# Optimization experiments

Measured on AMD Instinct MI355X. Metric: run time of the kernel, lower is better.

The kernel has to match this reference:

```python
import jax, jax.numpy as jnp
import numpy as np

LN_EPS = 1e-3

def setup_inputs() -> dict:
    key = jax.random.key(0)
    ks = jax.random.split(key, 3)
    B, H, W, C = 32, 64, 48, 256
    groups = 8
    d = C // groups
    x = jax.random.normal(ks[0], (B, H, W, C), dtype=jnp.float32)
    conv1x1_w = jax.random.normal(ks[1], (d, d), dtype=jnp.float32) * (1.0 / np.sqrt(d))
    conv1x1_b = jnp.zeros((d,), dtype=jnp.float32)
    conv3x3_w = jax.random.normal(ks[2], (3, 3, d, d), dtype=jnp.float32) * (1.0 / np.sqrt(9 * d))
    conv3x3_b = jnp.zeros((d,), dtype=jnp.float32)
    ln_gamma = jnp.ones((d,), dtype=jnp.float32)
    ln_beta = jnp.zeros((d,), dtype=jnp.float32)
    return {"x": x, "conv1x1_w": conv1x1_w, "conv1x1_b": conv1x1_b,
            "conv3x3_w": conv3x3_w, "conv3x3_b": conv3x3_b,
            "ln_gamma": ln_gamma, "ln_beta": ln_beta, "groups": groups}


def reference(x, conv1x1_w, conv1x1_b, conv3x3_w, conv3x3_b, ln_gamma, ln_beta, groups):
    B, H, W, C = x.shape
    g = groups
    d = C // g
    # group split: [B,H,W,C] -> [B*g, H, W, d]
    gx = x.reshape(B, H, W, g, d).transpose(0, 3, 1, 2, 4).reshape(B * g, H, W, d)
    # adaptive pools to (H,1) and (1,W) == mean over W / mean over H
    x_h = gx.mean(axis=2, keepdims=True)                 # [Bg,H,1,d]
    x_w = gx.mean(axis=1, keepdims=True)                 # [Bg,1,W,d]
    hw = jnp.concatenate([x_h, x_w.transpose(0, 2, 1, 3)], axis=1)  # [Bg,H+W,1,d]
    # conv1x1 == per-position linear over channels
    hw = jnp.einsum('bhwd,de->bhwe', hw, conv1x1_w) + conv1x1_b
    xh = jax.nn.sigmoid(hw[:, :H])                       # [Bg,H,1,d]
    xw = jax.nn.sigmoid(hw[:, H:].transpose(0, 2, 1, 3)) # [Bg,1,W,d]
    # LayerNorm over last axis
    y = gx * xh * xw
    mu = y.mean(axis=-1, keepdims=True)
    var = jnp.mean(jnp.square(y - mu), axis=-1, keepdims=True)
    x1 = (y - mu) * jax.lax.rsqrt(var + LN_EPS) * ln_gamma + ln_beta
    # conv3x3 SAME on grouped features
    x2 = jax.lax.conv_general_dilated(
        gx, conv3x3_w, window_strides=(1, 1), padding='SAME',
        dimension_numbers=('NHWC', 'HWIO', 'NHWC')) + conv3x3_b
    # channel softmax of GAP, cross matmuls -> spatial gate
    x11 = jax.nn.softmax(x1.mean(axis=(1, 2)), axis=-1)  # [Bg,d]
    x21 = jax.nn.softmax(x2.mean(axis=(1, 2)), axis=-1)  # [Bg,d]
    w1 = jnp.einsum('bd,bhwd->bhw', x11, x2)
    w2 = jnp.einsum('bd,bhwd->bhw', x21, x1)
    gate = jax.nn.sigmoid((w1 + w2)[..., None])          # [Bg,H,W,1]
    out = gx * gate
    out = out.reshape(B, g, H, W, d).transpose(0, 2, 3, 1, 4).reshape(B, H, W, C)
    return out
```

## Files before the change

### kernel.cpp

```cpp
#include <hip/hip_runtime.h>
#include <math.h>

#define B_ 32
#define H_ 64
#define W_ 48
#define C_ 256
#define G_ 8
#define D_ 32
#define BG_ (B_*G_)
#define LN_EPS_ 1e-3f
#define NPIX_ (H_*W_)

typedef short bf16x8 __attribute__((ext_vector_type(8)));
typedef float f32x4 __attribute__((ext_vector_type(4)));

__device__ __forceinline__ float sigmoidf_(float v) { return 1.0f / (1.0f + expf(-v)); }

__device__ __forceinline__ unsigned short f2bf(float f) {
    unsigned u = __float_as_uint(f);
    u = u + 0x7fffu + ((u >> 16) & 1u);
    return (unsigned short)(u >> 16);
}
__device__ __forceinline__ float bflo(unsigned u) { return __uint_as_float(u << 16); }
__device__ __forceinline__ float bfhi(unsigned u) { return __uint_as_float(u & 0xffff0000u); }

__global__ __launch_bounds__(256) void k0_prep(const float* __restrict__ w3,
                                               unsigned short* __restrict__ wbf)
{
    int i = blockIdx.x * 256 + threadIdx.x;
    if (i < 9 * D_ * D_) {
        int t = i >> 10;
        int rem = i & 1023;
        int e = rem >> 5, d = rem & 31;
        wbf[i] = f2bf(w3[((t << 5) + d) * D_ + e]);
    }
}

__global__ __launch_bounds__(256) void k1_means(const float* __restrict__ x,
                                                const float* __restrict__ w1,
                                                const float* __restrict__ b1,
                                                float* __restrict__ xh,
                                                float* __restrict__ xw)
{
    int bg = blockIdx.x;
    int b = bg >> 3, gi = bg & 7;
    const float* xp = x + (size_t)b * H_ * W_ * C_ + gi * D_;
    __shared__ float mh[H_][D_];
    __shared__ float mw[W_][D_];
    __shared__ float wls[D_ * D_];
    int t = threadIdx.x;
    int c = t & 31;
    int wg = t >> 5;
    for (int i = t; i < D_ * D_; i += 256) wls[i] = w1[i];
    for (int i = t; i < H_ * D_; i += 256) mh[i >> 5][i & 31] = 0.f;
    __syncthreads();

    float colp[6] = {0.f, 0.f, 0.f, 0.f, 0.f, 0.f};
    for (int h = 0; h < H_; ++h) {
        const float* row = xp + (size_t)h * W_ * C_;
        float rp = 0.f;
        #pragma unroll
        for (int j = 0; j < 6; ++j) {
            float v = row[(size_t)(wg * 6 + j) * C_ + c];
            rp += v;
            colp[j] += v;
        }
        rp += __shfl_xor(rp, 32);
        if ((t & 63) < 32) atomicAdd(&mh[h][c], rp);
    }
    #pragma unroll
    for (int j = 0; j < 6; ++j) mw[wg * 6 + j][c] = colp[j] * (1.0f / H_);
    __syncthreads();

    for (int i = t; i < (H_ + W_) * D_; i += 256) {
        int pos = i >> 5, e = i & 31;
        const float* m = (pos < H_) ? mh[pos] : mw[pos - H_];
        float scale = (pos < H_) ? (1.0f / W_) : 1.0f;
        float dot = 0.f;
        #pragma unroll
        for (int d = 0; d < D_; ++d) dot += m[d] * wls[d * D_ + e];
        float s = sigmoidf_(b1[e] + dot * scale);
        if (pos < H_) xh[((size_t)bg * H_ + pos) * D_ + e] = s;
        else          xw[((size_t)bg * W_ + (pos - H_)) * D_ + e] = s;
    }
}

#define SROWS 18
#define SPXL 50
#define ROWB (SPXL * 64)

__global__ __launch_bounds__(256) void k3_conv(const float* __restrict__ x,
                                               const unsigned short* __restrict__ wbf,
                                               const float* __restrict__ b3,
                                               const float* __restrict__ xh,
                                               const float* __restrict__ xw,
                                               const float* __restrict__ gamma,
                                               const float* __restrict__ beta,
                                               unsigned short* __restrict__ x2,
                                               float* __restrict__ s1,
                                               float* __restrict__ s2)
{
    __shared__ unsigned short sbuf[SROWS * SPXL * 32];
    int bi = blockIdx.x;
    int bg = bi >> 2;
    int h0 = (bi & 3) << 4;
    int b = bg >> 3, gi = bg & 7;
    const float* base = x + (size_t)b * H_ * W_ * C_ + gi * D_;
    int t = threadIdx.x;
    int lane = t & 63;
    int wv = t >> 6;

    const int e0 = lane & 15;
    const int ko = (lane >> 4) << 3;
    bf16x8 wf[9][2];
    #pragma unroll
    for (int tp = 0; tp < 9; ++tp)
        #pragma unroll
        for (int n = 0; n < 2; ++n)
            wf[tp][n] = *(const bf16x8*)(const void*)(wbf + (((tp << 5) + (n << 4) + e0) << 5) + ko);
    float be0 = b3[e0], be1 = b3[e0 + 16];

    if (t < SROWS * 2 * 4) {
        int r = t >> 3, side = (t >> 2) & 1, slot = t & 3;
        int px = side ? (SPXL - 1) : 0;
        int addr = r * ROWB + ((((px << 6) + (slot << 4))) ^ ((px & 7) << 4));
        *(uint4*)((char*)sbuf + addr) = make_uint4(0, 0, 0, 0);
    }

    const int NIDX = SROWS * 48 * 8;
    for (int i = t; i < NIDX; i += 256) {
        int r = i / 384;
        int rem = i - r * 384;
        int w = rem >> 3, c4 = rem & 7;
        int hh = h0 - 1 + r;
        unsigned u0 = 0, u1 = 0;
        if (hh >= 0 && hh < H_) {
            float4 v = *(const float4*)(base + ((size_t)hh * W_ + w) * C_ + (c4 << 2));
            u0 = (unsigned)f2bf(v.x) | ((unsigned)f2bf(v.y) << 16);
            u1 = (unsigned)f2bf(v.z) | ((unsigned)f2bf(v.w) << 16);
        }
        int px = w + 1;
        int addr = r * ROWB + ((((px << 6) + (c4 << 3))) ^ ((px & 7) << 4));
        *(uint2*)((char*)sbuf + addr) = make_uint2(u0, u1);
    }
    __syncthreads();

    float s2p0 = 0.f, s2p1 = 0.f;
    for (int q = 0; q < 4; ++q) {
        int r = (wv << 2) + q;
        int h = h0 + r;
        for (int m = 0; m < 3; ++m) {
            int w0 = m << 4;
            f32x4 acc0 = {be0, be0, be0, be0};
            f32x4 acc1 = {be1, be1, be1, be1};
            #pragma unroll
            for (int dh = 0; dh < 3; ++dh) {
                int srow = r + dh;
                #pragma unroll
                for (int dw = 0; dw < 3; ++dw) {
                    int px = w0 + (lane & 15) + dw;
                    int addr = srow * ROWB + ((((px << 6) + ((lane >> 4) << 4))) ^ ((px & 7) << 4));
                    bf16x8 a = *(const bf16x8*)(const void*)((const char*)sbuf + addr);
                    acc0 = __builtin_amdgcn_mfma_f32_16x16x32_bf16(a, wf[dh * 3 + dw][0], acc0, 0, 0, 0);
                    acc1 = __builtin_amdgcn_mfma_f32_16x16x32_bf16(a, wf[dh * 3 + dw][1], acc1, 0, 0, 0);
                }
            }
            #pragma unroll
            for (int rg = 0; rg < 4; ++rg) {
                int pw = w0 + ((lane >> 4) << 2) + rg;
                size_t off = (((size_t)bg * H_ + h) * W_ + pw) * D_;
                x2[off + e0]      = f2bf(acc0[rg]);
                x2[off + e0 + 16] = f2bf(acc1[rg]);
                s2p0 += acc0[rg];
                s2p1 += acc1[rg];
            }
        }
    }
    s2p0 += __shfl_xor(s2p0, 16); s2p0 += __shfl_xor(s2p0, 32);
    s2p1 += __shfl_xor(s2p1, 16); s2p1 += __shfl_xor(s2p1, 32);
    if (lane < 16) {
        atomicAdd(&s2[bg * D_ + e0], s2p0);
        atomicAdd(&s2[bg * D_ + e0 + 16], s2p1);
    }

    float s1p[32];
    #pragma unroll
    for (int c = 0; c < 32; ++c) s1p[c] = 0.f;
    #pragma unroll
    for (int pp = 0; pp < 3; ++pp) {
        int pl = t + (pp << 8);
        int r = pl / 48;
        int w = pl - r * 48;
        int srow = r + 1;
        int px = w + 1;
        float v[32];
        #pragma unroll
        for (int slot = 0; slot < 4; ++slot) {
            int addr = srow * ROWB + ((((px << 6) + (slot << 4))) ^ ((px & 7) << 4));
            uint4 u = *(const uint4*)((const char*)sbuf + addr);
            v[slot * 8 + 0] = bflo(u.x); v[slot * 8 + 1] = bfhi(u.x);
            v[slot * 8 + 2] = bflo(u.y); v[slot * 8 + 3] = bfhi(u.y);
            v[slot * 8 + 4] = bflo(u.z); v[slot * 8 + 5] = bfhi(u.z);
            v[slot * 8 + 6] = bflo(u.w); v[slot * 8 + 7] = bfhi(u.w);
        }
        const float4* ph4 = (const float4*)(xh + (((size_t)bg * H_) + h0 + r) * D_);
        const float4* pw4 = (const float4*)(xw + (((size_t)bg * W_) + w) * D_);
        float y[32];
        float mu = 0.f;
        #pragma unroll
        for (int c4 = 0; c4 < 8; ++c4) {
            float4 a = ph4[c4], bq = pw4[c4];
            y[4 * c4 + 0] = v[4 * c4 + 0] * a.x * bq.x;
            y[4 * c4 + 1] = v[4 * c4 + 1] * a.y * bq.y;
            y[4 * c4 + 2] = v[4 * c4 + 2] * a.z * bq.z;
            y[4 * c4 + 3] = v[4 * c4 + 3] * a.w * bq.w;
            mu += y[4 * c4 + 0] + y[4 * c4 + 1] + y[4 * c4 + 2] + y[4 * c4 + 3];
        }
        mu *= (1.0f / D_);
        float var = 0.f;
        #pragma unroll
        for (int c = 0; c < 32; ++c) { float dl = y[c] - mu; var += dl * dl; }
        var *= (1.0f / D_);
        float rs = rsqrtf(var + LN_EPS_);
        #pragma unroll
        for (int c4 = 0; c4 < 8; ++c4) {
            float4 gq = ((const float4*)gamma)[c4];
            float4 bt = ((const float4*)beta)[c4];
            s1p[4 * c4 + 0] += (y[4 * c4 + 0] - mu) * rs * gq.x + bt.x;
            s1p[4 * c4 + 1] += (y[4 * c4 + 1] - mu) * rs * gq.y + bt.y;
            s1p[4 * c4 + 2] += (y[4 * c4 + 2] - mu) * rs * gq.z + bt.z;
            s1p[4 * c4 + 3] += (y[4 * c4 + 3] - mu) * rs * gq.w + bt.w;
        }
    }
    #pragma unroll
    for (int c = 0; c < 32; ++c) {
        float vv = s1p[c];
        vv += __shfl_xor(vv, 1);  vv += __shfl_xor(vv, 2);  vv += __shfl_xor(vv, 4);
        vv += __shfl_xor(vv, 8);  vv += __shfl_xor(vv, 16); vv += __shfl_xor(vv, 32);
        s1p[c] = vv;
    }
    if (lane == 0) {
        #pragma unroll
        for (int c = 0; c < 32; ++c) atomicAdd(&s1[bg * D_ + c], s1p[c]);
    }
}

__global__ __launch_bounds__(64) void k4_softmax(const float* __restrict__ s1,
                                                 const float* __restrict__ s2,
                                                 float* __restrict__ x11,
                                                 float* __restrict__ x21)
{
    int bg = blockIdx.x;
    int lane = threadIdx.x;
    const float* s = (lane < 32) ? s1 : s2;
    float* o = (lane < 32) ? x11 : x21;
    int c = lane & 31;
    float v = s[bg * D_ + c] * (1.0f / (float)NPIX_);
    float m = v;
    m = fmaxf(m, __shfl_xor(m, 1));  m = fmaxf(m, __shfl_xor(m, 2));
    m = fmaxf(m, __shfl_xor(m, 4));  m = fmaxf(m, __shfl_xor(m, 8));
    m = fmaxf(m, __shfl_xor(m, 16));
    float e = expf(v - m);
    float sm = e;
    sm += __shfl_xor(sm, 1);  sm += __shfl_xor(sm, 2);
    sm += __shfl_xor(sm, 4);  sm += __shfl_xor(sm, 8);
    sm += __shfl_xor(sm, 16);
    o[bg * D_ + c] = e / sm;
}

__global__ __launch_bounds__(192) void k5_final(const float* __restrict__ x,
                                                const float* __restrict__ xh,
                                                const float* __restrict__ xw,
                                                const float* __restrict__ gamma,
                                                const float* __restrict__ beta,
                                                const unsigned short* __restrict__ x2,
                                                const float* __restrict__ x11,
                                                const float* __restrict__ x21,
                                                float* __restrict__ out)
{
    int bi = blockIdx.x;
    int bg = bi >> 4;
    int h0 = (bi & 15) << 2;
    int tid = threadIdx.x;
    int r = tid / W_;
    int w = tid % W_;
    int h = h0 + r;
    int b = bg >> 3, gi = bg & 7;
    size_t pixoff = (size_t)b * H_ * W_ * C_ + ((size_t)h * W_ + w) * C_ + gi * D_;

    const float4* vp  = (const float4*)(x + pixoff);
    const float4* xhp = (const float4*)(xh + ((size_t)bg * H_ + h) * D_);
    const float4* xwp = (const float4*)(xw + ((size_t)bg * W_ + w) * D_);

    float v[D_], y[D_];
    float mu = 0.f;
    #pragma unroll
    for (int q = 0; q < 8; ++q) {
        float4 tq = vp[q], a = xhp[q], bq = xwp[q];
        v[4 * q + 0] = tq.x; v[4 * q + 1] = tq.y; v[4 * q + 2] = tq.z; v[4 * q + 3] = tq.w;
        y[4 * q + 0] = tq.x * a.x * bq.x;
        y[4 * q + 1] = tq.y * a.y * bq.y;
        y[4 * q + 2] = tq.z * a.z * bq.z;
        y[4 * q + 3] = tq.w * a.w * bq.w;
        mu += y[4 * q + 0] + y[4 * q + 1] + y[4 * q + 2] + y[4 * q + 3];
    }
    mu *= (1.0f / D_);
    float var = 0.f;
    #pragma unroll
    for (int c = 0; c < D_; ++c) { float dl = y[c] - mu; var += dl * dl; }
    var *= (1.0f / D_);
    float rs = rsqrtf(var + LN_EPS_);

    const uint4* x2q = (const uint4*)(x2 + (((size_t)bg * H_ + h) * W_ + w) * D_);
    float w1 = 0.f, w2 = 0.f;
    #pragma unroll
    for (int j = 0; j < 4; ++j) {
        uint4 u = x2q[j];
        float xv[8];
        xv[0] = bflo(u.x); xv[1] = bfhi(u.x); xv[2] = bflo(u.y); xv[3] = bfhi(u.y);
        xv[4] = bflo(u.z); xv[5] = bfhi(u.z); xv[6] = bflo(u.w); xv[7] = bfhi(u.w);
        #pragma unroll
        for (int k = 0; k < 8; ++k) {
            int c = j * 8 + k;
            float x1v = (y[c] - mu) * rs * gamma[c] + beta[c];
            w1 += x11[bg * D_ + c] * xv[k];
            w2 += x21[bg * D_ + c] * x1v;
        }
    }
    float gate = sigmoidf_(w1 + w2);

    float4* op = (float4*)(out + pixoff);
    #pragma unroll
    for (int q = 0; q < 8; ++q) {
        float4 tq;
        tq.x = v[4 * q + 0] * gate; tq.y = v[4 * q + 1] * gate;
        tq.z = v[4 * q + 2] * gate; tq.w = v[4 * q + 3] * gate;
        op[q] = tq;
    }
}

extern "C" void kernel_launch(void* const* d_in, const int* in_sizes, int n_in,
                              void* d_out, int out_size, void* d_ws, size_t ws_size,
                              hipStream_t stream)
{
    const float* x     = (const float*)d_in[0];
    const float* w1    = (const float*)d_in[1];
    const float* b1    = (const float*)d_in[2];
    const float* w3    = (const float*)d_in[3];
    const float* b3    = (const float*)d_in[4];
    const float* gamma = (const float*)d_in[5];
    const float* beta  = (const float*)d_in[6];

    char* wsb = (char*)d_ws;
    unsigned short* x2  = (unsigned short*)wsb;
    float* xh  = (float*)(wsb + 50331648);
    float* xw  = (float*)(wsb + 52428800);
    float* s1  = (float*)(wsb + 54001664);
    float* s2  = (float*)(wsb + 54034432);
    float* x11 = (float*)(wsb + 54067200);
    float* x21 = (float*)(wsb + 54099968);
    unsigned short* wbf = (unsigned short*)(wsb + 54132736);

    hipMemsetAsync(s1, 0, 65536, stream);

    k0_prep<<<36, 256, 0, stream>>>(w3, wbf);
    k1_means<<<BG_, 256, 0, stream>>>(x, w1, b1, xh, xw);
    k3_conv<<<BG_ * 4, 256, 0, stream>>>(x, wbf, b3, xh, xw, gamma, beta, x2, s1, s2);
    k4_softmax<<<BG_, 64, 0, stream>>>(s1, s2, x11, x21);
    k5_final<<<BG_ * (H_ / 4), 192, 0, stream>>>(x, xh, xw, gamma, beta, x2, x11, x21,
                                                 (float*)d_out);
}
```

Measured before the change: 343.1 us.

## Stage bf16 copy of input in means kernel and reuse it in conv and final

The means kernel now writes a swizzled bf16 copy of each group's input. It also emits the row and column gates in bf16, using more threads and float4 loads. The conv kernel copies its tiles from that bf16 buffer straight into LDS with global_load_lds, using smaller 8-row tiles and masking at the edges instead of padding. The final kernel reads the bf16 input rather than the fp32 one. This cuts fp32 input reads in the later kernels, but the extra bf16 write costs traffic and the output gating now uses bf16-rounded inputs, which lowers precision.

```diff
diff --git a/kernel.cpp b/kernel.cpp
--- a/kernel.cpp
+++ b/kernel.cpp
@@ -10,6 +10,7 @@
 #define BG_ (B_*G_)
 #define LN_EPS_ 1e-3f
 #define NPIX_ (H_*W_)
+#define XROWB 3072
 
 typedef short bf16x8 __attribute__((ext_vector_type(8)));
 typedef float f32x4 __attribute__((ext_vector_type(4)));
@@ -23,6 +24,10 @@
 }
 __device__ __forceinline__ float bflo(unsigned u) { return __uint_as_float(u << 16); }
 __device__ __forceinline__ float bfhi(unsigned u) { return __uint_as_float(u & 0xffff0000u); }
+
+__device__ __forceinline__ int swz16(int px, int slot) {
+    return ((px << 6) + (slot << 4)) ^ ((px & 7) << 4);
+}
 
 __global__ __launch_bounds__(256) void k0_prep(const float* __restrict__ w3,
                                                unsigned short* __restrict__ wbf)
@@ -36,79 +41,103 @@
     }
 }
 
-__global__ __launch_bounds__(256) void k1_means(const float* __restrict__ x,
+__global__ __launch_bounds__(512) void k1_means(const float* __restrict__ x,
                                                 const float* __restrict__ w1,
                                                 const float* __restrict__ b1,
-                                                float* __restrict__ xh,
-                                                float* __restrict__ xw)
-{
+                                                unsigned short* __restrict__ xbf,
+                                                unsigned short* __restrict__ xhb,
+                                                unsigned short* __restrict__ xwb)
+{
+    __shared__ float mh[H_][D_];
+    __shared__ float mwp[8][W_][D_];
+    __shared__ float wls[D_ * D_];
     int bg = blockIdx.x;
-    int b = bg >> 3, gi = bg & 7;
-    const float* xp = x + (size_t)b * H_ * W_ * C_ + gi * D_;
-    __shared__ float mh[H_][D_];
-    __shared__ float mw[W_][D_];
-    __shared__ float wls[D_ * D_];
-    int t = threadIdx.x;
-    int c = t & 31;
-    int wg = t >> 5;
-    for (int i = t; i < D_ * D_; i += 256) wls[i] = w1[i];
-    for (int i = t; i < H_ * D_; i += 256) mh[i >> 5][i & 31] = 0.f;
-    __syncthreads();
-
-    float colp[6] = {0.f, 0.f, 0.f, 0.f, 0.f, 0.f};
-    for (int h = 0; h < H_; ++h) {
-        const float* row = xp + (size_t)h * W_ * C_;
-        float rp = 0.f;
-        #pragma unroll
-        for (int j = 0; j < 6; ++j) {
-            float v = row[(size_t)(wg * 6 + j) * C_ + c];
-            rp += v;
-            colp[j] += v;
-        }
-        rp += __shfl_xor(rp, 32);
-        if ((t & 63) < 32) atomicAdd(&mh[h][c], rp);
-    }
-    #pragma unroll
-    for (int j = 0; j < 6; ++j) mw[wg * 6 + j][c] = colp[j] * (1.0f / H_);
-    __syncthreads();
-
-    for (int i = t; i < (H_ + W_) * D_; i += 256) {
-        int pos = i >> 5, e = i & 31;
-        const float* m = (pos < H_) ? mh[pos] : mw[pos - H_];
-        float scale = (pos < H_) ? (1.0f / W_) : 1.0f;
-        float dot = 0.f;
-        #pragma unroll
-        for (int d = 0; d < D_; ++d) dot += m[d] * wls[d * D_ + e];
-        float s = sigmoidf_(b1[e] + dot * scale);
-        if (pos < H_) xh[((size_t)bg * H_ + pos) * D_ + e] = s;
-        else          xw[((size_t)bg * W_ + (pos - H_)) * D_ + e] = s;
-    }
-}
-
-#define SROWS 18
-#define SPXL 50
-#define ROWB (SPXL * 64)
-
-__global__ __launch_bounds__(256) void k3_conv(const float* __restrict__ x,
-                                               const unsigned short* __restrict__ wbf,
-                                               const float* __restrict__ b3,
-                                               const float* __restrict__ xh,
-                                               const float* __restrict__ xw,
-                                               const float* __restrict__ gamma,
-                                               const float* __restrict__ beta,
-                                               unsigned short* __restrict__ x2,
-                                               float* __restrict__ s1,
-                                               float* __restrict__ s2)
-{
-    __shared__ unsigned short sbuf[SROWS * SPXL * 32];
-    int bi = blockIdx.x;
-    int bg = bi >> 2;
-    int h0 = (bi & 3) << 4;
     int b = bg >> 3, gi = bg & 7;
     const float* base = x + (size_t)b * H_ * W_ * C_ + gi * D_;
     int t = threadIdx.x;
     int lane = t & 63;
     int wv = t >> 6;
+    int c4 = lane & 7;
+    int pxg = lane >> 3;
+
+    for (int i = t; i < D_ * D_; i += 512) wls[i] = w1[i];
+
+    float4 colp[6];
+    #pragma unroll
+    for (int j = 0; j < 6; ++j) colp[j] = make_float4(0.f, 0.f, 0.f, 0.f);
+
+    for (int i = 0; i < 8; ++i) {
+        int h = (wv << 3) + i;
+        const float* rowp = base + (size_t)h * W_ * C_;
+        char* xrow = (char*)xbf + (((size_t)bg << 6) + h) * XROWB;
+        float4 vj[6];
+        #pragma unroll
+        for (int j = 0; j < 6; ++j)
+            vj[j] = *(const float4*)(rowp + (size_t)(pxg + 8 * j) * C_ + (c4 << 2));
+        float4 rp = make_float4(0.f, 0.f, 0.f, 0.f);
+        #pragma unroll
+        for (int j = 0; j < 6; ++j) {
+            float4 v = vj[j];
+            int px = pxg + 8 * j;
+            unsigned u0 = (unsigned)f2bf(v.x) | ((unsigned)f2bf(v.y) << 16);
+            unsigned u1 = (unsigned)f2bf(v.z) | ((unsigned)f2bf(v.w) << 16);
+            int addr = (((px << 6) + (c4 << 3))) ^ ((px & 7) << 4);
+            *(uint2*)(xrow + addr) = make_uint2(u0, u1);
+            colp[j].x += v.x; colp[j].y += v.y; colp[j].z += v.z; colp[j].w += v.w;
+            rp.x += v.x; rp.y += v.y; rp.z += v.z; rp.w += v.w;
+        }
+        #pragma unroll
+        for (int s = 8; s <= 32; s <<= 1) {
+            rp.x += __shfl_xor(rp.x, s); rp.y += __shfl_xor(rp.y, s);
+            rp.z += __shfl_xor(rp.z, s); rp.w += __shfl_xor(rp.w, s);
+        }
+        if (lane < 8) *(float4*)&mh[h][c4 << 2] = rp;
+    }
+    #pragma unroll
+    for (int j = 0; j < 6; ++j)
+        *(float4*)&mwp[wv][pxg + 8 * j][c4 << 2] = colp[j];
+    __syncthreads();
+
+    for (int i = t; i < W_ * D_; i += 512) {
+        int px = i >> 5, c = i & 31;
+        float s = 0.f;
+        #pragma unroll
+        for (int v = 0; v < 8; ++v) s += mwp[v][px][c];
+        mwp[0][px][c] = s;
+    }
+    __syncthreads();
+
+    for (int i = t; i < (H_ + W_) * D_; i += 512) {
+        int pos = i >> 5, e = i & 31;
+        const float* m = (pos < H_) ? mh[pos] : mwp[0][pos - H_];
+        float scale = (pos < H_) ? (1.0f / W_) : (1.0f / H_);
+        float dot = 0.f;
+        #pragma unroll
+        for (int d = 0; d < D_; ++d) dot += m[d] * wls[d * D_ + e];
+        unsigned short s = f2bf(sigmoidf_(b1[e] + dot * scale));
+        if (pos < H_) xhb[(((size_t)bg << 6) + pos) * D_ + e] = s;
+        else          xwb[((size_t)bg * W_ + (pos - H_)) * D_ + e] = s;
+    }
+}
+
+__global__ __launch_bounds__(256, 4) void k3_conv(const unsigned short* __restrict__ xbf,
+                                                  const unsigned short* __restrict__ wbf,
+                                                  const float* __restrict__ b3,
+                                                  const unsigned short* __restrict__ xhb,
+                                                  const unsigned short* __restrict__ xwb,
+                                                  const float* __restrict__ gamma,
+                                                  const float* __restrict__ beta,
+                                                  unsigned short* __restrict__ x2,
+                                                  float* __restrict__ s1,
+                                                  float* __restrict__ s2)
+{
+    __shared__ unsigned short sbuf[10 * W_ * D_];
+    int bi = blockIdx.x;
+    int bg = bi >> 3;
+    int h0 = (bi & 7) << 3;
+    int t = threadIdx.x;
+    int lane = t & 63;
+    int wv = t >> 6;
 
     const int e0 = lane & 15;
     const int ko = (lane >> 4) << 3;
@@ -120,47 +149,51 @@
             wf[tp][n] = *(const bf16x8*)(const void*)(wbf + (((tp << 5) + (n << 4) + e0) << 5) + ko);
     float be0 = b3[e0], be1 = b3[e0 + 16];
 
-    if (t < SROWS * 2 * 4) {
-        int r = t >> 3, side = (t >> 2) & 1, slot = t & 3;
-        int px = side ? (SPXL - 1) : 0;
-        int addr = r * ROWB + ((((px << 6) + (slot << 4))) ^ ((px & 7) << 4));
-        *(uint4*)((char*)sbuf + addr) = make_uint4(0, 0, 0, 0);
-    }
-
-    const int NIDX = SROWS * 48 * 8;
-    for (int i = t; i < NIDX; i += 256) {
-        int r = i / 384;
-        int rem = i - r * 384;
-        int w = rem >> 3, c4 = rem & 7;
-        int hh = h0 - 1 + r;
-        unsigned u0 = 0, u1 = 0;
-        if (hh >= 0 && hh < H_) {
-            float4 v = *(const float4*)(base + ((size_t)hh * W_ + w) * C_ + (c4 << 2));
-            u0 = (unsigned)f2bf(v.x) | ((unsigned)f2bf(v.y) << 16);
-            u1 = (unsigned)f2bf(v.z) | ((unsigned)f2bf(v.w) << 16);
-        }
-        int px = w + 1;
-        int addr = r * ROWB + ((((px << 6) + (c4 << 3))) ^ ((px & 7) << 4));
-        *(uint2*)((char*)sbuf + addr) = make_uint2(u0, u1);
-    }
+    int sA = (h0 == 0) ? 1 : 0;
+    int sB = (h0 == 56) ? 8 : 9;
+    const char* src = (const char*)xbf + (((size_t)bg << 6) + (h0 - 1 + sA)) * XROWB;
+    char* ldsb = (char*)sbuf + sA * XROWB;
+    int nch = (sB - sA + 1) * 3;
+    for (int ch = wv; ch < nch; ch += 4) {
+        __builtin_amdgcn_global_load_lds(
+            (const __attribute__((address_space(1))) unsigned*)(const void*)(src + (ch << 10) + (lane << 4)),
+            (__attribute__((address_space(3))) unsigned*)(void*)(ldsb + (ch << 10)),
+            16, 0, 0);
+    }
+    if (h0 == 0 && t < 192)  *(uint4*)((char*)sbuf + (t << 4)) = make_uint4(0, 0, 0, 0);
+    if (h0 == 56 && t < 192) *(uint4*)((char*)sbuf + 9 * XROWB + (t << 4)) = make_uint4(0, 0, 0, 0);
     __syncthreads();
 
+    int swz9[9]; bool inv9[9];
+    #pragma unroll
+    for (int m = 0; m < 3; ++m)
+        #pragma unroll
+        for (int dw = 0; dw < 3; ++dw) {
+            int pxi = (m << 4) + (lane & 15) + dw - 1;
+            int pxc = pxi < 0 ? 0 : (pxi > 47 ? 47 : pxi);
+            swz9[m * 3 + dw] = swz16(pxc, lane >> 4);
+            inv9[m * 3 + dw] = (pxi != pxc);
+        }
+    const bf16x8 z8 = {0, 0, 0, 0, 0, 0, 0, 0};
+
     float s2p0 = 0.f, s2p1 = 0.f;
-    for (int q = 0; q < 4; ++q) {
-        int r = (wv << 2) + q;
+    for (int q = 0; q < 2; ++q) {
+        int r = (wv << 1) + q;
         int h = h0 + r;
+        #pragma unroll
         for (int m = 0; m < 3; ++m) {
             int w0 = m << 4;
             f32x4 acc0 = {be0, be0, be0, be0};
             f32x4 acc1 = {be1, be1, be1, be1};
             #pragma unroll
             for (int dh = 0; dh < 3; ++dh) {
-                int srow = r + dh;
+                int srowB = (r + dh) * XROWB;
                 #pragma unroll
                 for (int dw = 0; dw < 3; ++dw) {
-                    int px = w0 + (lane & 15) + dw;
-                    int addr = srow * ROWB + ((((px << 6) + ((lane >> 4) << 4))) ^ ((px & 7) << 4));
-                    bf16x8 a = *(const bf16x8*)(const void*)((const char*)sbuf + addr);
+                    bf16x8 a = *(const bf16x8*)(const void*)((const char*)sbuf + srowB + swz9[m * 3 + dw]);
+                    if ((m == 0 && dw == 0) || (m == 2 && dw == 2)) {
+                        if (inv9[m * 3 + dw]) a = z8;
+                    }
                     acc0 = __builtin_amdgcn_mfma_f32_16x16x32_bf16(a, wf[dh * 3 + dw][0], acc0, 0, 0, 0);
                     acc1 = __builtin_amdgcn_mfma_f32_16x16x32_bf16(a, wf[dh * 3 + dw][1], acc1, 0, 0, 0);
                 }
@@ -186,35 +219,32 @@
     float s1p[32];
     #pragma unroll
     for (int c = 0; c < 32; ++c) s1p[c] = 0.f;
-    #pragma unroll
-    for (int pp = 0; pp < 3; ++pp) {
-        int pl = t + (pp << 8);
-        int r = pl / 48;
-        int w = pl - r * 48;
-        int srow = r + 1;
-        int px = w + 1;
-        float v[32];
-        #pragma unroll
-        for (int slot = 0; slot < 4; ++slot) {
-            int addr = srow * ROWB + ((((px << 6) + (slot << 4))) ^ ((px & 7) << 4));
-            uint4 u = *(const uint4*)((const char*)sbuf + addr);
-            v[slot * 8 + 0] = bflo(u.x); v[slot * 8 + 1] = bfhi(u.x);
-            v[slot * 8 + 2] = bflo(u.y); v[slot * 8 + 3] = bfhi(u.y);
-            v[slot * 8 + 4] = bflo(u.z); v[slot * 8 + 5] = bfhi(u.z);
-            v[slot * 8 + 6] = bflo(u.w); v[slot * 8 + 7] = bfhi(u.w);
-        }
-        const float4* ph4 = (const float4*)(xh + (((size_t)bg * H_) + h0 + r) * D_);
-        const float4* pw4 = (const float4*)(xw + (((size_t)bg * W_) + w) * D_);
+    for (int pl = t; pl < 8 * W_; pl += 256) {
+        int r = pl / W_;
+        int w = pl - r * W_;
+        int srowB = (r + 1) * XROWB;
+        const uint4* ph4 = (const uint4*)(xhb + (((size_t)bg << 6) + h0 + r) * D_);
+        const uint4* pw4 = (const uint4*)(xwb + ((size_t)bg * W_ + w) * D_);
         float y[32];
         float mu = 0.f;
         #pragma unroll
-        for (int c4 = 0; c4 < 8; ++c4) {
-            float4 a = ph4[c4], bq = pw4[c4];
-            y[4 * c4 + 0] = v[4 * c4 + 0] * a.x * bq.x;
-            y[4 * c4 + 1] = v[4 * c4 + 1] * a.y * bq.y;
-            y[4 * c4 + 2] = v[4 * c4 + 2] * a.z * bq.z;
-            y[4 * c4 + 3] = v[4 * c4 + 3] * a.w * bq.w;
-            mu += y[4 * c4 + 0] + y[4 * c4 + 1] + y[4 * c4 + 2] + y[4 * c4 + 3];
+        for (int j = 0; j < 4; ++j) {
+            uint4 uv = *(const uint4*)((const char*)sbuf + srowB + swz16(w, j));
+            uint4 uh = ph4[j];
+            uint4 uw = pw4[j];
+            float vv[8], ah[8], aw[8];
+            vv[0]=bflo(uv.x); vv[1]=bfhi(uv.x); vv[2]=bflo(uv.y); vv[3]=bfhi(uv.y);
+            vv[4]=bflo(uv.z); vv[5]=bfhi(uv.z); vv[6]=bflo(uv.w); vv[7]=bfhi(uv.w);
+            ah[0]=bflo(uh.x); ah[1]=bfhi(uh.x); ah[2]=bflo(uh.y); ah[3]=bfhi(uh.y);
+            ah[4]=bflo(uh.z); ah[5]=bfhi(uh.z); ah[6]=bflo(uh.w); ah[7]=bfhi(uh.w);
+            aw[0]=bflo(uw.x); aw[1]=bfhi(uw.x); aw[2]=bflo(uw.y); aw[3]=bfhi(uw.y);
+            aw[4]=bflo(uw.z); aw[5]=bfhi(uw.z); aw[6]=bflo(uw.w); aw[7]=bfhi(uw.w);
+            #pragma unroll
+            for (int k = 0; k < 8; ++k) {
+                float yy = vv[k] * ah[k] * aw[k];
+                y[j * 8 + k] = yy;
+                mu += yy;
+            }
         }
         mu *= (1.0f / D_);
         float var = 0.f;
@@ -268,9 +298,9 @@
     o[bg * D_ + c] = e / sm;
 }
 
-__global__ __launch_bounds__(192) void k5_final(const float* __restrict__ x,
-                                                const float* __restrict__ xh,
-                                                const float* __restrict__ xw,
+__global__ __launch_bounds__(192) void k5_final(const unsigned short* __restrict__ xbf,
+                                                const unsigned short* __restrict__ xhb,
+                                                const unsigned short* __restrict__ xwb,
                                                 const float* __restrict__ gamma,
                                                 const float* __restrict__ beta,
                                                 const unsigned short* __restrict__ x2,
@@ -286,23 +316,31 @@
     int w = tid % W_;
     int h = h0 + r;
     int b = bg >> 3, gi = bg & 7;
-    size_t pixoff = (size_t)b * H_ * W_ * C_ + ((size_t)h * W_ + w) * C_ + gi * D_;
-
-    const float4* vp  = (const float4*)(x + pixoff);
-    const float4* xhp = (const float4*)(xh + ((size_t)bg * H_ + h) * D_);
-    const float4* xwp = (const float4*)(xw + ((size_t)bg * W_ + w) * D_);
-
-    float v[D_], y[D_];
+
+    const char* xrow = (const char*)xbf + (((size_t)bg << 6) + h) * XROWB;
+    const uint4* ph4 = (const uint4*)(xhb + (((size_t)bg << 6) + h) * D_);
+    const uint4* pw4 = (const uint4*)(xwb + ((size_t)bg * W_ + w) * D_);
+
+    float v[32], y[32];
     float mu = 0.f;
     #pragma unroll
-    for (int q = 0; q < 8; ++q) {
-        float4 tq = vp[q], a = xhp[q], bq = xwp[q];
-        v[4 * q + 0] = tq.x; v[4 * q + 1] = tq.y; v[4 * q + 2] = tq.z; v[4 * q + 3] = tq.w;
-        y[4 * q + 0] = tq.x * a.x * bq.x;
-        y[4 * q + 1] = tq.y * a.y * bq.y;
-        y[4 * q + 2] = tq.z * a.z * bq.z;
-        y[4 * q + 3] = tq.w * a.w * bq.w;
-        mu += y[4 * q + 0] + y[4 * q + 1] + y[4 * q + 2] + y[4 * q + 3];
+    for (int j = 0; j < 4; ++j) {
+        uint4 uv = *(const uint4*)(xrow + swz16(w, j));
+        uint4 uh = ph4[j];
+        uint4 uw = pw4[j];
+        float ah[8], aw[8];
+        v[j*8+0]=bflo(uv.x); v[j*8+1]=bfhi(uv.x); v[j*8+2]=bflo(uv.y); v[j*8+3]=bfhi(uv.y);
+        v[j*8+4]=bflo(uv.z); v[j*8+5]=bfhi(uv.z); v[j*8+6]=bflo(uv.w); v[j*8+7]=bfhi(uv.w);
+        ah[0]=bflo(uh.x); ah[1]=bfhi(uh.x); ah[2]=bflo(uh.y); ah[3]=bfhi(uh.y);
+        ah[4]=bflo(uh.z); ah[5]=bfhi(uh.z); ah[6]=bflo(uh.w); ah[7]=bfhi(uh.w);
+        aw[0]=bflo(uw.x); aw[1]=bfhi(uw.x); aw[2]=bflo(uw.y); aw[3]=bfhi(uw.y);
+        aw[4]=bflo(uw.z); aw[5]=bfhi(uw.z); aw[6]=bflo(uw.w); aw[7]=bfhi(uw.w);
+        #pragma unroll
+        for (int k = 0; k < 8; ++k) {
+            float yy = v[j * 8 + k] * ah[k] * aw[k];
+            y[j * 8 + k] = yy;
+            mu += yy;
+        }
     }
     mu *= (1.0f / D_);
     float var = 0.f;
@@ -329,6 +367,7 @@
     }
     float gate = sigmoidf_(w1 + w2);
 
+    size_t pixoff = (size_t)b * H_ * W_ * C_ + ((size_t)h * W_ + w) * C_ + gi * D_;
     float4* op = (float4*)(out + pixoff);
     #pragma unroll
     for (int q = 0; q < 8; ++q) {
@@ -353,20 +392,21 @@
 
     char* wsb = (char*)d_ws;
     unsigned short* x2  = (unsigned short*)wsb;
-    float* xh  = (float*)(wsb + 50331648);
-    float* xw  = (float*)(wsb + 52428800);
-    float* s1  = (float*)(wsb + 54001664);
-    float* s2  = (float*)(wsb + 54034432);
-    float* x11 = (float*)(wsb + 54067200);
-    float* x21 = (float*)(wsb + 54099968);
-    unsigned short* wbf = (unsigned short*)(wsb + 54132736);
+    unsigned short* xbf = (unsigned short*)(wsb + 50331648);
+    unsigned short* xhb = (unsigned short*)(wsb + 100663296);
+    unsigned short* xwb = (unsigned short*)(wsb + 101711872);
+    float* s1  = (float*)(wsb + 102498304);
+    float* s2  = (float*)(wsb + 102531072);
+    float* x11 = (float*)(wsb + 102563840);
+    float* x21 = (float*)(wsb + 102596608);
+    unsigned short* wbf = (unsigned short*)(wsb + 102629376);
 
     hipMemsetAsync(s1, 0, 65536, stream);
 
     k0_prep<<<36, 256, 0, stream>>>(w3, wbf);
-    k1_means<<<BG_, 256, 0, stream>>>(x, w1, b1, xh, xw);
-    k3_conv<<<BG_ * 4, 256, 0, stream>>>(x, wbf, b3, xh, xw, gamma, beta, x2, s1, s2);
+    k1_means<<<BG_, 512, 0, stream>>>(x, w1, b1, xbf, xhb, xwb);
+    k3_conv<<<BG_ * 8, 256, 0, stream>>>(xbf, wbf, b3, xhb, xwb, gamma, beta, x2, s1, s2);
     k4_softmax<<<BG_, 64, 0, stream>>>(s1, s2, x11, x21);
-    k5_final<<<BG_ * (H_ / 4), 192, 0, stream>>>(x, xh, xw, gamma, beta, x2, x11, x21,
+    k5_final<<<BG_ * (H_ / 4), 192, 0, stream>>>(xbf, xhb, xwb, gamma, beta, x2, x11, x21,
                                                  (float*)d_out);
 }
```

Result: slower. 362.5 us (+5.6%).
